# Kernel optimization log

Measured on AMD Instinct MI355X. Metric: run time of the kernel, lower is better.

## Reference

```python
import jax, jax.numpy as jnp
import numpy as np
import math

N_HEADS = 16
EPS = 1e-6


def rmsnorm(x, w):
    xf = x.astype(jnp.float32)
    n = xf * jax.lax.rsqrt(jnp.mean(xf * xf, axis=-1, keepdims=True) + EPS)
    return n.astype(x.dtype) * w


def setup_inputs() -> dict:
    key = jax.random.key(0)
    ks = jax.random.split(key, 8)
    B, T, C, Hf = 1, 4096, 1024, 4096
    s = lambda fan_in: 1.0 / math.sqrt(fan_in)
    return {
        "x": jax.random.normal(ks[0], (B, T, C), jnp.float32),
        "attn_norm_w": jnp.ones((C,), jnp.float32),
        "ffn_norm_w": jnp.ones((C,), jnp.float32),
        "c_attn_w": jax.random.normal(ks[1], (3 * C, C), jnp.float32) * s(C),
        "c_proj_w": jax.random.normal(ks[2], (C, C), jnp.float32) * s(C),
        "w1": jax.random.normal(ks[3], (Hf, C), jnp.float32) * s(C),
        "w2": jax.random.normal(ks[4], (C, Hf), jnp.float32) * s(Hf),
        "w3": jax.random.normal(ks[5], (Hf, C), jnp.float32) * s(C),
    }


def attention(x, c_attn_w, c_proj_w):
    B, T, C = x.shape
    hd = C // N_HEADS
    qkv = x @ c_attn_w.T  # [B,T,3C]
    q, k, v = jnp.split(qkv, 3, axis=-1)
    q = q.reshape(B, T, N_HEADS, hd).transpose(0, 2, 1, 3)  # [B,H,T,hd]
    k = k.reshape(B, T, N_HEADS, hd).transpose(0, 2, 1, 3)
    v = v.reshape(B, T, N_HEADS, hd).transpose(0, 2, 1, 3)
    att = jnp.einsum('bhqd,bhkd->bhqk', q, k) * (1.0 / math.sqrt(hd))
    mask = jnp.tril(jnp.ones((T, T), bool))  # causal
    att = jnp.where(mask, att, -jnp.inf)
    att = jax.nn.softmax(att, axis=-1)
    y = jnp.einsum('bhqk,bhkd->bhqd', att, v)
    y = y.transpose(0, 2, 1, 3).reshape(B, T, C)
    return y @ c_proj_w.T


def ffn(x, w1, w2, w3):
    return (jax.nn.silu(x @ w1.T) * (x @ w3.T)) @ w2.T


def reference(x, attn_norm_w, ffn_norm_w, c_attn_w, c_proj_w, w1, w2, w3):
    x = x + attention(rmsnorm(x, attn_norm_w), c_attn_w, c_proj_w)
    x = x + ffn(rmsnorm(x, ffn_norm_w), w1, w2, w3)
    return x
```

## Files before the change

kernel.cpp:

```cpp
#include <hip/hip_runtime.h>
#include <hip/hip_bf16.h>

typedef __hip_bfloat16 bf16;
typedef __bf16 bf16r;
typedef bf16r bf16x8 __attribute__((ext_vector_type(8)));
typedef bf16r bf16x4 __attribute__((ext_vector_type(4)));
typedef float f32x4 __attribute__((ext_vector_type(4)));

#define T_SEQ 4096
#define C_DIM 1024
#define LD_QKV 3072
#define MB(x) ((size_t)(x) << 20)
#define SCL 0.18033688011112042f

static __device__ __forceinline__ unsigned short f2bf(float f) {
    bf16 h = (bf16)f;
    return *reinterpret_cast<unsigned short*>(&h);
}

__global__ __launch_bounds__(256) void cvt_w(const float* __restrict__ src, size_t eoff,
                                             ushort4* __restrict__ dst, int n4) {
    int i = blockIdx.x * 256 + threadIdx.x;
    const int stride = gridDim.x * 256;
    const float4* s = (const float4*)(src + eoff);
    for (; i < n4; i += stride) {
        float4 v = s[i];
        ushort4 o;
        o.x = f2bf(v.x); o.y = f2bf(v.y); o.z = f2bf(v.z); o.w = f2bf(v.w);
        dst[i] = o;
    }
}

__global__ __launch_bounds__(256) void cvt_w2h(const float* __restrict__ src, int coff,
                                               ushort4* __restrict__ dst) {
    const int i = blockIdx.x * 256 + threadIdx.x;
    const int row = i >> 9;
    const int c4 = i & 511;
    float4 v = *(const float4*)(src + (size_t)row * 4096 + coff + c4 * 4);
    ushort4 o;
    o.x = f2bf(v.x); o.y = f2bf(v.y); o.z = f2bf(v.z); o.w = f2bf(v.w);
    dst[i] = o;
}

__global__ __launch_bounds__(256) void rmsnorm_k(const float* __restrict__ x,
                                                 const float* __restrict__ w,
                                                 bf16* __restrict__ out) {
    const int row = blockIdx.x;
    const int tid = threadIdx.x;
    const float* xr = x + (size_t)row * C_DIM;
    float v[4];
    float ss = 0.f;
#pragma unroll
    for (int i = 0; i < 4; i++) { v[i] = xr[tid * 4 + i]; ss += v[i] * v[i]; }
#pragma unroll
    for (int off = 32; off; off >>= 1) ss += __shfl_xor(ss, off);
    __shared__ float red[4];
    if ((tid & 63) == 0) red[tid >> 6] = ss;
    __syncthreads();
    const float tot = red[0] + red[1] + red[2] + red[3];
    const float scale = rsqrtf(tot * (1.0f / C_DIM) + 1e-6f);
#pragma unroll
    for (int i = 0; i < 4; i++) {
        const int c = tid * 4 + i;
        out[(size_t)row * C_DIM + c] = (bf16)(v[i] * scale * w[c]);
    }
}

template <int RESID, int OUTF32>
__global__ __launch_bounds__(256) void gemm128(const bf16* __restrict__ A, int lda,
                                               const bf16* __restrict__ B, int ldb,
                                               const void* __restrict__ resid,
                                               void* __restrict__ out,
                                               int N, int K) {
    __shared__ __align__(16) bf16r As[128 * 32];
    __shared__ __align__(16) bf16r Bs[128 * 32];
    const int tid = threadIdx.x;
    const int w = tid >> 6, lane = tid & 63;
    const int c = lane & 15, qd = lane >> 4;
    const int wm = w >> 1, wn = w & 1;
    const int mbase = blockIdx.y * 128;
    const int nbase = blockIdx.x * 128;

    const int srow = lane >> 2, schk = lane & 3;
    const bf16* gA = A + (size_t)(mbase + w * 32 + srow) * lda + schk * 8;
    const bf16* gB = B + (size_t)(nbase + w * 32 + srow) * ldb + schk * 8;

    f32x4 acc[4][4] = {};

    for (int k0 = 0; k0 < K; k0 += 32) {
        __syncthreads();
#pragma unroll
        for (int s = 0; s < 2; s++) {
            __builtin_amdgcn_global_load_lds(
                (const __attribute__((address_space(1))) void*)(gA + (size_t)(s * 16) * lda + k0),
                (__attribute__((address_space(3))) void*)&As[(w * 32 + s * 16) * 32], 16, 0, 0);
            __builtin_amdgcn_global_load_lds(
                (const __attribute__((address_space(1))) void*)(gB + (size_t)(s * 16) * ldb + k0),
                (__attribute__((address_space(3))) void*)&Bs[(w * 32 + s * 16) * 32], 16, 0, 0);
        }
        __syncthreads();

        bf16x8 a[4], b[4];
#pragma unroll
        for (int i = 0; i < 4; i++)
            a[i] = *(const bf16x8*)&As[(wm * 64 + i * 16 + c) * 32 + qd * 8];
#pragma unroll
        for (int j = 0; j < 4; j++)
            b[j] = *(const bf16x8*)&Bs[(wn * 64 + j * 16 + c) * 32 + qd * 8];
#pragma unroll
        for (int i = 0; i < 4; i++)
#pragma unroll
            for (int j = 0; j < 4; j++)
                acc[i][j] = __builtin_amdgcn_mfma_f32_16x16x32_bf16(a[i], b[j], acc[i][j], 0, 0, 0);
    }

#pragma unroll
    for (int i = 0; i < 4; i++) {
#pragma unroll
        for (int j = 0; j < 4; j++) {
            const int col = nbase + wn * 64 + j * 16 + c;
#pragma unroll
            for (int reg = 0; reg < 4; reg++) {
                const int row = mbase + wm * 64 + i * 16 + qd * 4 + reg;
                const size_t idx = (size_t)row * N + col;
                float v = acc[i][j][reg];
                if (RESID == 2) v += ((const float*)resid)[idx];
                if (RESID == 3) {
                    const float a1 = (float)((const bf16*)resid)[idx];
                    v = (a1 / (1.0f + __expf(-a1))) * v;
                }
                if (OUTF32)
                    ((float*)out)[idx] = v;
                else
                    ((bf16*)out)[idx] = (bf16)v;
            }
        }
    }
}

__global__ __launch_bounds__(256) void build_tr(const bf16* __restrict__ qkv,
                                                bf16* __restrict__ dst, int soff) {
    const int h = blockIdx.y;
    const int tb = blockIdx.x;
    __shared__ bf16 tile[64][65];
    const int tx = threadIdx.x & 63;
    const int ty = threadIdx.x >> 6;
    for (int rr = ty; rr < 64; rr += 4)
        tile[rr][tx] = qkv[(size_t)(tb * 64 + rr) * LD_QKV + soff + h * 64 + tx];
    __syncthreads();
    for (int rr = ty; rr < 64; rr += 4)
        dst[((size_t)h * 64 + rr) * T_SEQ + tb * 64 + tx] = tile[tx][rr];
}

__global__ __launch_bounds__(256, 3) void attn_mfma(const bf16* __restrict__ qkv,
                                                    const bf16* __restrict__ VT,
                                                    bf16* __restrict__ y) {
    __shared__ __align__(16) bf16r Ks[128][64];
    __shared__ __align__(16) bf16r VTs[64][128];
    __shared__ __align__(16) bf16r Ps[4][16][128];

    const int tid  = threadIdx.x;
    const int w    = tid >> 6;
    const int lane = tid & 63;
    const int c    = lane & 15;
    const int qd   = lane >> 4;
    const int id   = blockIdx.x;
    const int h    = id & 15;
    const int qt   = id >> 4;
    const int qb   = (qt & 1) ? (63 - (qt >> 1)) : (qt >> 1);
    const int qrow = qb * 64 + w * 16 + c;
    const int sw   = c & 7;

    bf16x8 qf[2];
    {
        const bf16* qp = qkv + (size_t)qrow * LD_QKV + h * 64;
        qf[0] = *(const bf16x8*)(qp + qd * 8);
        qf[1] = *(const bf16x8*)(qp + 32 + qd * 8);
    }

    const int skr = tid >> 3, sch = tid & 7;
    const int svr = tid >> 4, svch = tid & 15;

    f32x4 O[4] = {};
    float m_i = -1e30f, l_i = 0.f;
    const int nkb = (qb >> 1) + 1;

    bf16x8 kreg[4], vreg[4];
#pragma unroll
    for (int ii = 0; ii < 4; ii++) {
        const int kr = skr + ii * 32;
        kreg[ii] = *(const bf16x8*)(qkv + (size_t)kr * LD_QKV + C_DIM + h * 64 + sch * 8);
        const int vr = svr + ii * 16;
        vreg[ii] = *(const bf16x8*)(VT + ((size_t)h * 64 + vr) * T_SEQ + svch * 8);
    }

    for (int kb = 0; kb < nkb; kb++) {
        __syncthreads();
#pragma unroll
        for (int ii = 0; ii < 4; ii++) {
            const int kr = skr + ii * 32;
            *(bf16x8*)&Ks[kr][(sch ^ (kr & 7)) * 8] = kreg[ii];
            const int vr = svr + ii * 16;
            *(bf16x8*)&VTs[vr][(svch ^ (vr & 7)) * 8] = vreg[ii];
        }
        __syncthreads();
        if (kb + 1 < nkb) {
#pragma unroll
            for (int ii = 0; ii < 4; ii++) {
                const int kr = skr + ii * 32;
                kreg[ii] = *(const bf16x8*)(qkv + (size_t)((kb + 1) * 128 + kr) * LD_QKV + C_DIM + h * 64 + sch * 8);
                const int vr = svr + ii * 16;
                vreg[ii] = *(const bf16x8*)(VT + ((size_t)h * 64 + vr) * T_SEQ + (kb + 1) * 128 + svch * 8);
            }
        }

        f32x4 ST[8];
#pragma unroll
        for (int kt = 0; kt < 8; kt++) {
            f32x4 z = {};
#pragma unroll
            for (int ks = 0; ks < 2; ks++) {
                bf16x8 kf = *(const bf16x8*)&Ks[kt * 16 + c][((ks * 4 + qd) ^ sw) * 8];
                z = __builtin_amdgcn_mfma_f32_16x16x32_bf16(kf, qf[ks], z, 0, 0, 0);
            }
            ST[kt] = z;
        }

        if (kb == nkb - 1) {
#pragma unroll
            for (int kt = 0; kt < 8; kt++)
#pragma unroll
                for (int r = 0; r < 4; r++) {
                    float s = ST[kt][r] * SCL;
                    if (kb * 128 + kt * 16 + qd * 4 + r > qrow) s = -1e30f;
                    ST[kt][r] = s;
                }
        } else {
#pragma unroll
            for (int kt = 0; kt < 8; kt++)
#pragma unroll
                for (int r = 0; r < 4; r++) ST[kt][r] *= SCL;
        }

        float mb = -1e30f;
#pragma unroll
        for (int kt = 0; kt < 8; kt++)
#pragma unroll
            for (int r = 0; r < 4; r++) mb = fmaxf(mb, ST[kt][r]);
        mb = fmaxf(mb, __shfl_xor(mb, 16));
        mb = fmaxf(mb, __shfl_xor(mb, 32));

        bf16x4 pv[8];
        float rs = 0.f;
        if (__all(mb - m_i <= 8.0f)) {
#pragma unroll
            for (int kt = 0; kt < 8; kt++)
#pragma unroll
                for (int r = 0; r < 4; r++) {
                    const float p = exp2f(ST[kt][r] - m_i);
                    pv[kt][r] = (bf16r)p;
                    rs += p;
                }
            rs += __shfl_xor(rs, 16);
            rs += __shfl_xor(rs, 32);
            l_i += rs;
        } else {
            const float mnew = fmaxf(m_i, mb);
            const float alpha = exp2f(m_i - mnew);
#pragma unroll
            for (int kt = 0; kt < 8; kt++)
#pragma unroll
                for (int r = 0; r < 4; r++) {
                    const float p = exp2f(ST[kt][r] - mnew);
                    pv[kt][r] = (bf16r)p;
                    rs += p;
                }
            rs += __shfl_xor(rs, 16);
            rs += __shfl_xor(rs, 32);
            l_i = l_i * alpha + rs;
            m_i = mnew;
#pragma unroll
            for (int dt = 0; dt < 4; dt++)
#pragma unroll
                for (int r = 0; r < 4; r++) O[dt][r] *= alpha;
        }

#pragma unroll
        for (int kt = 0; kt < 8; kt++) {
            const int phys = (kt * 2 + (qd >> 1)) ^ sw;
            *(bf16x4*)&Ps[w][c][phys * 8 + (qd & 1) * 4] = pv[kt];
        }

#pragma unroll
        for (int ks = 0; ks < 4; ks++) {
            bf16x8 pf = *(const bf16x8*)&Ps[w][c][((ks * 4 + qd) ^ sw) * 8];
#pragma unroll
            for (int dt = 0; dt < 4; dt++) {
                bf16x8 vf = *(const bf16x8*)&VTs[dt * 16 + c][((ks * 4 + qd) ^ sw) * 8];
                O[dt] = __builtin_amdgcn_mfma_f32_16x16x32_bf16(vf, pf, O[dt], 0, 0, 0);
            }
        }
    }

    const float inv_l = 1.0f / l_i;
#pragma unroll
    for (int dt = 0; dt < 4; dt++) {
        bf16x4 ov;
#pragma unroll
        for (int r = 0; r < 4; r++) ov[r] = (bf16r)(O[dt][r] * inv_l);
        *(bf16x4*)(y + (size_t)qrow * C_DIM + h * 64 + dt * 16 + qd * 4) = ov;
    }
}

extern "C" void kernel_launch(void* const* d_in, const int* in_sizes, int n_in,
                              void* d_out, int out_size, void* d_ws, size_t ws_size,
                              hipStream_t stream) {
    const float* x        = (const float*)d_in[0];
    const float* attn_w   = (const float*)d_in[1];
    const float* ffn_w    = (const float*)d_in[2];
    const float* c_attn_w = (const float*)d_in[3];
    const float* c_proj_w = (const float*)d_in[4];
    const float* w1       = (const float*)d_in[5];
    const float* w2       = (const float*)d_in[6];
    const float* w3       = (const float*)d_in[7];
    float* xmid = (float*)d_out;

    char* ws = (char*)d_ws;
    bf16* cwA = (bf16*)(ws);
    bf16* cwP = (bf16*)(ws + MB(6));
    bf16* rms = (bf16*)(ws + MB(8));
    bf16* qkv = (bf16*)(ws + MB(16));
    bf16* VT  = (bf16*)(ws + MB(40));
    bf16* y   = (bf16*)(ws + MB(48));
    bf16* w1h = (bf16*)(ws + MB(16));
    bf16* w3h = (bf16*)(ws + MB(20));
    bf16* w2h = (bf16*)(ws + MB(24));
    bf16* h1h = (bf16*)(ws + MB(28));

    cvt_w<<<512, 256, 0, stream>>>(c_attn_w, 0, (ushort4*)cwA, 3072 * 1024 / 4);
    cvt_w<<<512, 256, 0, stream>>>(c_proj_w, 0, (ushort4*)cwP, 1024 * 1024 / 4);
    rmsnorm_k<<<T_SEQ, 256, 0, stream>>>(x, attn_w, rms);
    gemm128<0, 0><<<dim3(24, 32), 256, 0, stream>>>(rms, C_DIM, cwA, C_DIM, nullptr, qkv, 3072, 1024);
    build_tr<<<dim3(64, 16), 256, 0, stream>>>(qkv, VT, 2 * C_DIM);
    attn_mfma<<<1024, 256, 0, stream>>>(qkv, VT, y);
    gemm128<2, 1><<<dim3(8, 32), 256, 0, stream>>>(y, C_DIM, cwP, C_DIM, x, xmid, 1024, 1024);
    rmsnorm_k<<<T_SEQ, 256, 0, stream>>>(xmid, ffn_w, rms);
    for (int hh = 0; hh < 2; hh++) {
        cvt_w<<<512, 256, 0, stream>>>(w1, (size_t)hh * 2048 * 1024, (ushort4*)w1h, 2048 * 1024 / 4);
        gemm128<0, 0><<<dim3(16, 32), 256, 0, stream>>>(rms, C_DIM, w1h, C_DIM, nullptr, h1h, 2048, 1024);
        cvt_w<<<512, 256, 0, stream>>>(w3, (size_t)hh * 2048 * 1024, (ushort4*)w3h, 2048 * 1024 / 4);
        gemm128<3, 0><<<dim3(16, 32), 256, 0, stream>>>(rms, C_DIM, w3h, C_DIM, h1h, h1h, 2048, 1024);
        cvt_w2h<<<2048, 256, 0, stream>>>(w2, hh * 2048, (ushort4*)w2h);
        gemm128<2, 1><<<dim3(8, 32), 256, 0, stream>>>(h1h, 2048, w2h, 2048, xmid, xmid, 1024, 2048);
    }
}
```

Baseline: 582.8 us.

## Double-buffer attention K/V tiles via direct global-to-LDS async loads

Replaces the register-staged K and V^T prefetch in the attention kernel with __builtin_amdgcn_global_load_lds writes into double-buffered shared memory, dropping one __syncthreads per key block. The next block's load is issued into the alternate buffer while the current one is computed on, with the XOR swizzle applied on the global source address instead. This frees the prefetch registers and the LDS store instructions, but doubles K/V LDS use and removes the 3-blocks-per-CU launch bound, which may lower occupancy.

```diff
diff --git a/kernel.cpp b/kernel.cpp
--- a/kernel.cpp
+++ b/kernel.cpp
@@ -152,11 +152,11 @@
         dst[((size_t)h * 64 + rr) * T_SEQ + tb * 64 + tx] = tile[tx][rr];
 }
 
-__global__ __launch_bounds__(256, 3) void attn_mfma(const bf16* __restrict__ qkv,
-                                                    const bf16* __restrict__ VT,
-                                                    bf16* __restrict__ y) {
-    __shared__ __align__(16) bf16r Ks[128][64];
-    __shared__ __align__(16) bf16r VTs[64][128];
+__global__ __launch_bounds__(256) void attn_mfma(const bf16* __restrict__ qkv,
+                                                 const bf16* __restrict__ VT,
+                                                 bf16* __restrict__ y) {
+    __shared__ __align__(16) bf16r Ks[2][128][64];
+    __shared__ __align__(16) bf16r VTs[2][64][128];
     __shared__ __align__(16) bf16r Ps[4][16][128];
 
     const int tid  = threadIdx.x;
@@ -178,41 +178,39 @@
         qf[1] = *(const bf16x8*)(qp + 32 + qd * 8);
     }
 
-    const int skr = tid >> 3, sch = tid & 7;
-    const int svr = tid >> 4, svch = tid & 15;
+    const int k_ri = lane >> 3, k_pc = lane & 7;
+    const int v_ri = lane >> 4, v_pc = lane & 15;
+
+    auto stage = [&](int kb, int buf) {
+#pragma unroll
+        for (int ii = 0; ii < 4; ii++) {
+            const int grp = w * 4 + ii;
+            const int kr = grp * 8 + k_ri;
+            const int kch = k_pc ^ (kr & 7);
+            __builtin_amdgcn_global_load_lds(
+                (const __attribute__((address_space(1))) void*)
+                    (qkv + (size_t)(kb * 128 + kr) * LD_QKV + C_DIM + h * 64 + kch * 8),
+                (__attribute__((address_space(3))) void*)&Ks[buf][grp * 8][0], 16, 0, 0);
+            const int vr = grp * 4 + v_ri;
+            const int vch = v_pc ^ (vr & 7);
+            __builtin_amdgcn_global_load_lds(
+                (const __attribute__((address_space(1))) void*)
+                    (VT + ((size_t)h * 64 + vr) * T_SEQ + kb * 128 + vch * 8),
+                (__attribute__((address_space(3))) void*)&VTs[buf][grp * 4][0], 16, 0, 0);
+        }
+    };
 
     f32x4 O[4] = {};
     float m_i = -1e30f, l_i = 0.f;
     const int nkb = (qb >> 1) + 1;
 
-    bf16x8 kreg[4], vreg[4];
-#pragma unroll
-    for (int ii = 0; ii < 4; ii++) {
-        const int kr = skr + ii * 32;
-        kreg[ii] = *(const bf16x8*)(qkv + (size_t)kr * LD_QKV + C_DIM + h * 64 + sch * 8);
-        const int vr = svr + ii * 16;
-        vreg[ii] = *(const bf16x8*)(VT + ((size_t)h * 64 + vr) * T_SEQ + svch * 8);
-    }
-
+    stage(0, 0);
+
+    int cur = 0;
     for (int kb = 0; kb < nkb; kb++) {
+        asm volatile("s_waitcnt vmcnt(0)" ::: "memory");
         __syncthreads();
-#pragma unroll
-        for (int ii = 0; ii < 4; ii++) {
-            const int kr = skr + ii * 32;
-            *(bf16x8*)&Ks[kr][(sch ^ (kr & 7)) * 8] = kreg[ii];
-            const int vr = svr + ii * 16;
-            *(bf16x8*)&VTs[vr][(svch ^ (vr & 7)) * 8] = vreg[ii];
-        }
-        __syncthreads();
-        if (kb + 1 < nkb) {
-#pragma unroll
-            for (int ii = 0; ii < 4; ii++) {
-                const int kr = skr + ii * 32;
-                kreg[ii] = *(const bf16x8*)(qkv + (size_t)((kb + 1) * 128 + kr) * LD_QKV + C_DIM + h * 64 + sch * 8);
-                const int vr = svr + ii * 16;
-                vreg[ii] = *(const bf16x8*)(VT + ((size_t)h * 64 + vr) * T_SEQ + (kb + 1) * 128 + svch * 8);
-            }
-        }
+        if (kb + 1 < nkb) stage(kb + 1, cur ^ 1);
 
         f32x4 ST[8];
 #pragma unroll
@@ -220,7 +218,7 @@
             f32x4 z = {};
 #pragma unroll
             for (int ks = 0; ks < 2; ks++) {
-                bf16x8 kf = *(const bf16x8*)&Ks[kt * 16 + c][((ks * 4 + qd) ^ sw) * 8];
+                bf16x8 kf = *(const bf16x8*)&Ks[cur][kt * 16 + c][((ks * 4 + qd) ^ sw) * 8];
                 z = __builtin_amdgcn_mfma_f32_16x16x32_bf16(kf, qf[ks], z, 0, 0, 0);
             }
             ST[kt] = z;
@@ -296,10 +294,11 @@
             bf16x8 pf = *(const bf16x8*)&Ps[w][c][((ks * 4 + qd) ^ sw) * 8];
 #pragma unroll
             for (int dt = 0; dt < 4; dt++) {
-                bf16x8 vf = *(const bf16x8*)&VTs[dt * 16 + c][((ks * 4 + qd) ^ sw) * 8];
+                bf16x8 vf = *(const bf16x8*)&VTs[cur][dt * 16 + c][((ks * 4 + qd) ^ sw) * 8];
                 O[dt] = __builtin_amdgcn_mfma_f32_16x16x32_bf16(vf, pf, O[dt], 0, 0, 0);
             }
         }
+        cur ^= 1;
     }
 
     const float inv_l = 1.0f / l_i;
```

Result: no change. 579.0 us (-0.7%).
